# Performance work log

Hardware: AMD Instinct MI355X
Metric: run time of the kernel (lower is better)

## Reference

```python
import jax, jax.numpy as jnp
import numpy as np

B, T, OMNI_D, STATIC_D = 128, 1024, 32, 16
H = 64            # hidden // 2 (per-direction GRU size)
HID = 128         # hidden
PHYS_LEN, N_PHYS = 432, 5


def _gelu(x):
    return jax.nn.gelu(x, approximate=False)  # torch GELU default = exact erf


def _ln(x, g, b, eps=1e-5):
    m = jnp.mean(x, -1, keepdims=True)
    v = jnp.var(x, -1, keepdims=True)
    return (x - m) / jnp.sqrt(v + eps) * g + b


def _gru_layer(x, Wih, Whh, bih, bhh, reverse):
    # PyTorch GRU cell math; x: [B,T,D] -> (outputs [B,T,H], h_final [B,H])
    Hh = Whh.shape[1]
    gi = jnp.einsum('btd,gd->btg', x, Wih) + bih  # precompute input projections
    if reverse:
        gi = gi[:, ::-1]
    gi = jnp.swapaxes(gi, 0, 1)  # [T,B,3H]
    h0 = jnp.zeros((x.shape[0], Hh), x.dtype)

    def step(h, g):
        gh = h @ Whh.T + bhh
        r = jax.nn.sigmoid(g[:, :Hh] + gh[:, :Hh])
        z = jax.nn.sigmoid(g[:, Hh:2 * Hh] + gh[:, Hh:2 * Hh])
        n = jnp.tanh(g[:, 2 * Hh:] + r * gh[:, 2 * Hh:])
        hn = (1 - z) * n + z * h
        return hn, hn

    hT, ys = jax.lax.scan(step, h0, gi)
    ys = jnp.swapaxes(ys, 0, 1)
    if reverse:
        ys = ys[:, ::-1]
    return ys, hT


def _conv1d(x, W, b, pad, dil):
    y = jax.lax.conv_general_dilated(x, W, (1,), [(pad, pad)], rhs_dilation=(dil,),
                                     dimension_numbers=('NCH', 'OIH', 'NCH'))
    return y + b[None, :, None]


def setup_inputs():
    key = jax.random.key(0)
    ks = iter(jax.random.split(key, 64))

    def rn(shape, s=0.05):
        return jax.random.normal(next(ks), shape, jnp.float32) * s

    inp = {
        'omni_seq': rn((B, T, OMNI_D), 1.0),
        'static_x': rn((B, STATIC_D), 1.0),
        'phys': rn((B, N_PHYS, PHYS_LEN), 1.0),
    }
    for l, d_in in (('l0', OMNI_D), ('l1', 2 * H)):
        for dr in ('f', 'b'):
            inp[f'gru_Wih_{l}{dr}'] = rn((3 * H, d_in))
            inp[f'gru_Whh_{l}{dr}'] = rn((3 * H, H))
            inp[f'gru_bih_{l}{dr}'] = rn((3 * H,))
            inp[f'gru_bhh_{l}{dr}'] = rn((3 * H,))
    inp['sm_W'] = rn((H, STATIC_D)); inp['sm_b'] = rn((H,))
    inp['sm_ln_g'] = jnp.ones((H,), jnp.float32); inp['sm_ln_b'] = jnp.zeros((H,), jnp.float32)
    inp['gate_W'] = rn((N_PHYS, H)); inp['gate_b'] = rn((N_PHYS,))
    inp['attn_in_W'] = rn((3 * N_PHYS, N_PHYS)); inp['attn_in_b'] = rn((3 * N_PHYS,))
    inp['attn_out_W'] = rn((N_PHYS, N_PHYS)); inp['attn_out_b'] = rn((N_PHYS,))
    for i, ksz in ((1, 3), (2, 5), (3, 9)):
        inp[f'conv{i}_W'] = rn((HID // 4, N_PHYS, ksz)); inp[f'conv{i}_b'] = rn((HID // 4,))
    FUSED = HID + H + 3 * (HID // 4)  # 288
    inp['head_ln_g'] = jnp.ones((FUSED,), jnp.float32); inp['head_ln_b'] = jnp.zeros((FUSED,), jnp.float32)
    inp['head_W1'] = rn((HID, FUSED)); inp['head_b1'] = rn((HID,))
    inp['head_W2'] = rn((PHYS_LEN, HID)); inp['head_b2'] = rn((PHYS_LEN,))
    return inp


def reference(omni_seq, static_x, phys,
              gru_Wih_l0f, gru_Whh_l0f, gru_bih_l0f, gru_bhh_l0f,
              gru_Wih_l0b, gru_Whh_l0b, gru_bih_l0b, gru_bhh_l0b,
              gru_Wih_l1f, gru_Whh_l1f, gru_bih_l1f, gru_bhh_l1f,
              gru_Wih_l1b, gru_Whh_l1b, gru_bih_l1b, gru_bhh_l1b,
              sm_W, sm_b, sm_ln_g, sm_ln_b, gate_W, gate_b,
              attn_in_W, attn_in_b, attn_out_W, attn_out_b,
              conv1_W, conv1_b, conv2_W, conv2_b, conv3_W, conv3_b,
              head_ln_g, head_ln_b, head_W1, head_b1, head_W2, head_b2):
    # --- bidirectional 2-layer GRU (eval mode: dropout off) ---
    y0f, _ = _gru_layer(omni_seq, gru_Wih_l0f, gru_Whh_l0f, gru_bih_l0f, gru_bhh_l0f, False)
    y0b, _ = _gru_layer(omni_seq, gru_Wih_l0b, gru_Whh_l0b, gru_bih_l0b, gru_bhh_l0b, True)
    x1 = jnp.concatenate([y0f, y0b], -1)
    _, hf = _gru_layer(x1, gru_Wih_l1f, gru_Whh_l1f, gru_bih_l1f, gru_bhh_l1f, False)
    _, hb = _gru_layer(x1, gru_Wih_l1b, gru_Whh_l1b, gru_bih_l1b, gru_bhh_l1b, True)
    omni_embed = jnp.concatenate([hf, hb], -1)  # h_omni[-2] ++ h_omni[-1], [B,128]
    # --- static MLP ---
    static_embed = _ln(_gelu(static_x @ sm_W.T + sm_b), sm_ln_g, sm_ln_b)  # [B,64]
    # --- gating on phys channels ---
    gates = jax.nn.sigmoid(static_embed @ gate_W.T + gate_b)[..., None]  # [B,5,1]
    p = phys * gates  # [B,5,432]
    # --- tiny MHA: embed_dim=5, 5 heads, head_dim=1 -> scale = 1/sqrt(1) = 1 ---
    pt = jnp.swapaxes(p, 1, 2)  # [B,432,5]
    qkv = pt @ attn_in_W.T + attn_in_b
    E = N_PHYS
    q, k, v = qkv[..., :E], qkv[..., E:2 * E], qkv[..., 2 * E:]
    scores = jnp.einsum('bih,bjh->bhij', q, k)  # [B,5,432,432]
    attn = jax.nn.softmax(scores, -1)
    ao = jnp.einsum('bhij,bjh->bih', attn, v)
    ao = ao @ attn_out_W.T + attn_out_b  # out_proj
    p = jnp.swapaxes(ao, 1, 2)  # [B,5,432]
    # --- dilated conv branches + GELU + adaptive avg pool (= mean over length) ---
    c1 = _gelu(_conv1d(p, conv1_W, conv1_b, 1, 1)).mean(-1)
    c2 = _gelu(_conv1d(p, conv2_W, conv2_b, 2, 2)).mean(-1)
    c3 = _gelu(_conv1d(p, conv3_W, conv3_b, 4, 4)).mean(-1)
    fused = jnp.concatenate([omni_embed, static_embed, c1, c2, c3], 1)  # [B,288]
    h = _ln(fused, head_ln_g, head_ln_b)
    h = _gelu(h @ head_W1.T + head_b1)  # dropout off in eval
    return h @ head_W2.T + head_b2  # [B,432]
```

## Files before the change

kernel.cpp:

```cpp
#include <hip/hip_runtime.h>
#include <stdint.h>

#define B_ 128
#define T_ 1024
#define BT_ (B_*T_)
#define H_ 64
#define G_ 192
#define PL_ 432
#define NP_ 5
#define FUSED_ 288
#define N_IN 41
#define NSTATIC 128

typedef unsigned short u16;
typedef __attribute__((ext_vector_type(8))) short bf16x8;
typedef __attribute__((ext_vector_type(4))) float f32x4;
typedef _Float16 h2 __attribute__((ext_vector_type(2)));
typedef _Float16 h8 __attribute__((ext_vector_type(8)));

__device__ inline float bf2f(u16 u){ union{float f; unsigned int i;} c; c.i = ((unsigned int)u)<<16; return c.f; }
__device__ inline u16 f2bf(float f){ unsigned int u = __float_as_uint(f); unsigned int r = (u + 0x7fffu + ((u>>16)&1u))>>16; return (u16)r; }
__device__ inline _Float16 bf2h(u16 u){ return (_Float16)bf2f(u); }
__device__ inline float sigm(float x){ return 1.f/(1.f+__expf(-x)); }
__device__ inline float tanh_(float x){ float t = __expf(fminf(fmaxf(2.f*x,-30.f),30.f)); return (t-1.f)/(t+1.f); }
__device__ inline float gelu_(float x){ return 0.5f*x*(1.f + erff(x*0.70710678118654752f)); }
__device__ inline float wredsum(float v){
  #pragma unroll
  for(int o=32;o>0;o>>=1) v += __shfl_xor(v,o);
  return v;
}

#if __has_builtin(__builtin_amdgcn_fdot2)
__device__ inline float dot2(h2 a, h2 b, float c){ return __builtin_amdgcn_fdot2(a, b, c, false); }
#else
__device__ inline float dot2(h2 a, h2 b, float c){ return c + (float)a.x*(float)b.x + (float)a.y*(float)b.y; }
#endif

struct CvtArgs {
  const void* src[N_IN];
  unsigned dstOff[N_IN];
  unsigned cnt[N_IN];
  unsigned blkStart[N_IN+1];
};

__global__ __launch_bounds__(256) void convert_k(CvtArgs a, u16* __restrict__ dst){
  const bool isbf = (((const u16*)a.src[21])[0] == 0x3F80u);
  int b = blockIdx.x;
  int lo = 0, hi = N_IN;
  while (hi - lo > 1){ int mid = (lo+hi)>>1; if (a.blkStart[mid] <= (unsigned)b) lo = mid; else hi = mid; }
  const int i = lo;
  const unsigned lb = (unsigned)b - a.blkStart[i];
  const unsigned n = a.cnt[i];
  u16* d = dst + a.dstOff[i];
  if (isbf){
    const u16* s = (const u16*)a.src[i];
    #pragma unroll
    for(int e=0;e<8;e++){ unsigned idx = lb*2048u + e*256u + threadIdx.x; if (idx < n) d[idx] = s[idx]; }
  } else {
    const float* s = (const float*)a.src[i];
    #pragma unroll
    for(int e=0;e<8;e++){ unsigned idx = lb*2048u + e*256u + threadIdx.x; if (idx < n) d[idx] = f2bf(s[idx]); }
  }
}

__global__ __launch_bounds__(256) void gi_gemm0(const void* __restrict__ Araw,
    const u16* __restrict__ Wf, const u16* __restrict__ Wb,
    const u16* __restrict__ biasF, const u16* __restrict__ biasB,
    u16* __restrict__ out, const u16* __restrict__ detect)
{
  const bool isbf = (detect[0] == 0x3F80u);
  const int wv = threadIdx.x >> 6, lane = threadIdx.x & 63;
  const int l15 = lane & 15, quad = lane >> 4;
  const size_t mBase = (size_t)blockIdx.x*64 + wv*16;

  bf16x8 afr;
  if (isbf){
    afr = *(const bf16x8*)((const u16*)Araw + (mBase + l15)*32 + quad*8);
  } else {
    const float* af = (const float*)Araw + (mBase + l15)*32 + quad*8;
    float4 f0 = *(const float4*)af;
    float4 f1 = *(const float4*)(af+4);
    union { bf16x8 v; u16 e[8]; } u_;
    u_.e[0]=f2bf(f0.x); u_.e[1]=f2bf(f0.y); u_.e[2]=f2bf(f0.z); u_.e[3]=f2bf(f0.w);
    u_.e[4]=f2bf(f1.x); u_.e[5]=f2bf(f1.y); u_.e[6]=f2bf(f1.z); u_.e[7]=f2bf(f1.w);
    afr = u_.v;
  }

  #pragma unroll
  for(int half=0; half<2; ++half){
    const u16* W    = half ? Wb : Wf;
    const u16* bias = half ? biasB : biasF;
    u16* o = out + (size_t)half * BT_ * G_;
    for(int nt=0; nt<12; ++nt){
      int n = nt*16 + l15;
      f32x4 acc = {0.f,0.f,0.f,0.f};
      bf16x8 bfr = *(const bf16x8*)(W + n*32 + quad*8);
      acc = __builtin_amdgcn_mfma_f32_16x16x32_bf16(bfr, afr, acc, 0,0,0);
      ushort4 bb = *(const ushort4*)(bias + nt*16 + quad*4);
      ushort4 pk;
      pk.x = f2bf(acc[0] + bf2f(bb.x));
      pk.y = f2bf(acc[1] + bf2f(bb.y));
      pk.z = f2bf(acc[2] + bf2f(bb.z));
      pk.w = f2bf(acc[3] + bf2f(bb.w));
      *(ushort4*)(o + (mBase + l15)*G_ + nt*16 + quad*4) = pk;
    }
  }
}

__global__ __launch_bounds__(64)
__attribute__((amdgpu_waves_per_eu(1,1)))
void recur(const u16* __restrict__ gi,
    const u16* __restrict__ WhF, const u16* __restrict__ WhB,
    const u16* __restrict__ bhF, const u16* __restrict__ bhB,
    u16* __restrict__ y_x1, float* __restrict__ hfin, int layer)
{
  const int chain = blockIdx.x;
  const int dir = chain >> 7;
  const int b = chain & 127;
  const int j = threadIdx.x;
  const u16* Wh = dir ? WhB : WhF;
  const u16* bh = dir ? bhB : bhF;

  h2 wr[32], wz[32], wn[32];
  #pragma unroll
  for(int k8=0;k8<8;k8++){
    uint4 q;
    q = *(const uint4*)(Wh + (size_t)j*64 + k8*8);
    wr[4*k8+0] = (h2){bf2h((u16)(q.x&0xffffu)), bf2h((u16)(q.x>>16))};
    wr[4*k8+1] = (h2){bf2h((u16)(q.y&0xffffu)), bf2h((u16)(q.y>>16))};
    wr[4*k8+2] = (h2){bf2h((u16)(q.z&0xffffu)), bf2h((u16)(q.z>>16))};
    wr[4*k8+3] = (h2){bf2h((u16)(q.w&0xffffu)), bf2h((u16)(q.w>>16))};
    q = *(const uint4*)(Wh + (size_t)(64+j)*64 + k8*8);
    wz[4*k8+0] = (h2){bf2h((u16)(q.x&0xffffu)), bf2h((u16)(q.x>>16))};
    wz[4*k8+1] = (h2){bf2h((u16)(q.y&0xffffu)), bf2h((u16)(q.y>>16))};
    wz[4*k8+2] = (h2){bf2h((u16)(q.z&0xffffu)), bf2h((u16)(q.z>>16))};
    wz[4*k8+3] = (h2){bf2h((u16)(q.w&0xffffu)), bf2h((u16)(q.w>>16))};
    q = *(const uint4*)(Wh + (size_t)(128+j)*64 + k8*8);
    wn[4*k8+0] = (h2){bf2h((u16)(q.x&0xffffu)), bf2h((u16)(q.x>>16))};
    wn[4*k8+1] = (h2){bf2h((u16)(q.y&0xffffu)), bf2h((u16)(q.y>>16))};
    wn[4*k8+2] = (h2){bf2h((u16)(q.z&0xffffu)), bf2h((u16)(q.z>>16))};
    wn[4*k8+3] = (h2){bf2h((u16)(q.w&0xffffu)), bf2h((u16)(q.w>>16))};
  }
  const float bhr = bf2f(bh[j]), bhz = bf2f(bh[64+j]), bhn = bf2f(bh[128+j]);

  __shared__ __align__(16) u16 giLds[2][3072];
  __shared__ _Float16 hSf[64];
  h8* hS8 = (h8*)hSf;
  hSf[j] = (_Float16)0.f;

  const u16* giC = gi + (size_t)chain * T_ * G_;

  auto issue_chunk = [&](int c, int buf){
    int tbase = dir ? (1008 - c*16) : (c*16);
    const u16* src = giC + (size_t)tbase*G_ + j*8;
    u16* dst = &giLds[buf][0];
    #pragma unroll
    for(int i=0;i<6;i++){
      __builtin_amdgcn_global_load_lds(
        (const __attribute__((address_space(1))) void*)(src + i*512),
        (__attribute__((address_space(3))) void*)(dst + i*512), 16, 0, 0);
    }
  };

  issue_chunk(0, 0);

  float h = 0.f;
  for(int c=0; c<64; ++c){
    asm volatile("s_waitcnt vmcnt(0)" ::: "memory");
    if (c < 63) issue_chunk(c+1, (c+1)&1);
    const u16* gbuf = &giLds[c&1][0];
    #pragma unroll 2
    for(int ls=0; ls<16; ++ls){
      int row = dir ? (15-ls) : ls;
      const u16* rowp = gbuf + row*G_;
      float r0=bhr, r1=0.f, z0=bhz, z1=0.f, n0=bhn, n1=0.f;
      #pragma unroll
      for(int k=0;k<8;k++){
        h8 hv = hS8[k];
        h2 p0 = __builtin_shufflevector(hv, hv, 0, 1);
        h2 p1 = __builtin_shufflevector(hv, hv, 2, 3);
        h2 p2 = __builtin_shufflevector(hv, hv, 4, 5);
        h2 p3 = __builtin_shufflevector(hv, hv, 6, 7);
        r0 = dot2(wr[4*k+0], p0, r0); r1 = dot2(wr[4*k+1], p1, r1);
        r0 = dot2(wr[4*k+2], p2, r0); r1 = dot2(wr[4*k+3], p3, r1);
        z0 = dot2(wz[4*k+0], p0, z0); z1 = dot2(wz[4*k+1], p1, z1);
        z0 = dot2(wz[4*k+2], p2, z0); z1 = dot2(wz[4*k+3], p3, z1);
        n0 = dot2(wn[4*k+0], p0, n0); n1 = dot2(wn[4*k+1], p1, n1);
        n0 = dot2(wn[4*k+2], p2, n0); n1 = dot2(wn[4*k+3], p3, n1);
      }
      float gr = bf2f(rowp[j]), gz = bf2f(rowp[64+j]), gn = bf2f(rowp[128+j]);

      float r  = sigm(gr + (r0+r1));
      float z  = sigm(gz + (z0+z1));
      float nn = tanh_(gn + r*(n0+n1));
      h = (1.f - z)*nn + z*h;

      hSf[j] = (_Float16)h;

      if (layer == 0){
        int s = c*16 + ls;
        int t = dir ? (T_-1-s) : s;
        y_x1[((size_t)b*T_ + t)*128 + dir*64 + j] = f2bf(h);
      }
    }
  }
  if (layer == 1) hfin[b*FUSED_ + dir*64 + j] = h;
}

template<int KS, int DIL, int PAD>
__device__ inline void do_conv(const float* pS, const u16* Wc, const u16* bc,
                               float* fused, int b, int o, int p, int cslot)
{
  const int Lout = PL_ + 2*PAD - DIL*(KS-1);
  float w[5][KS];
  #pragma unroll
  for(int i=0;i<5;i++)
    #pragma unroll
    for(int t=0;t<KS;t++) w[i][t] = bf2f(Wc[(o*5+i)*KS + t]);
  float bias = bf2f(bc[o]);
  float acc = 0.f;
  for(int l=p; l<Lout; l+=8){
    float s = bias;
    #pragma unroll
    for(int t=0;t<KS;t++){
      int idx = l - PAD + t*DIL;
      if (idx >= 0 && idx < PL_){
        #pragma unroll
        for(int i=0;i<5;i++) s += w[i][t]*pS[i*PL_ + idx];
      }
    }
    acc += gelu_(s);
  }
  #pragma unroll
  for(int off=1;off<8;off<<=1) acc += __shfl_xor(acc,off);
  if (p == 0) fused[b*FUSED_ + 192 + cslot*32 + o] = acc/(float)Lout;
}

__device__ void static_body(int b, int tid,
   const u16* sx, const u16* smW, const u16* smb,
   const u16* lng, const u16* lnb, const u16* gW, const u16* gb,
   const void* physRaw, const u16* aW, const u16* ab,
   const u16* oW, const u16* ob,
   const u16* W1c, const u16* b1c, const u16* W2c, const u16* b2c,
   const u16* W3c, const u16* b3c,
   float* fused, bool isbf)
{
  __shared__ float qS[15*PL_];
  __shared__ float aoS[PL_*5];
  __shared__ float gS[5];
  __shared__ float redS[40];
  __shared__ float kmS[5], knS[5];

  if (tid < 64){
    int j = tid;
    float acc = bf2f(smb[j]);
    #pragma unroll
    for(int k=0;k<16;k++) acc += bf2f(sx[b*16+k])*bf2f(smW[j*16+k]);
    float xg = gelu_(acc);
    float m = wredsum(xg)*(1.f/64.f);
    float d = xg - m;
    float v = wredsum(d*d)*(1.f/64.f);
    float se = d*rsqrtf(v+1e-5f)*bf2f(lng[j]) + bf2f(lnb[j]);
    fused[b*FUSED_ + 128 + j] = se;
    #pragma unroll
    for(int i=0;i<5;i++){
      float p = se*bf2f(gW[i*64+j]);
      float s = wredsum(p);
      if (j == 0) gS[i] = sigm(s + bf2f(gb[i]));
    }
  }
  __syncthreads();

  for(int l=tid; l<PL_; l+=256){
    float pv[5];
    #pragma unroll
    for(int i=0;i<5;i++){
      size_t idx = ((size_t)b*5+i)*PL_ + l;
      float pr = isbf ? bf2f(((const u16*)physRaw)[idx]) : ((const float*)physRaw)[idx];
      pv[i] = pr * gS[i];
    }
    #pragma unroll
    for(int c=0;c<15;c++){
      float a = bf2f(ab[c]);
      #pragma unroll
      for(int i=0;i<5;i++) a += pv[i]*bf2f(aW[c*5+i]);
      qS[c*PL_ + l] = a;
    }
  }
  __syncthreads();

  float mx[5], mn[5];
  #pragma unroll
  for(int h=0;h<5;h++){ mx[h]=-1e30f; mn[h]=1e30f; }
  for(int jj=tid; jj<PL_; jj+=256){
    #pragma unroll
    for(int h=0;h<5;h++){ float kv=qS[(5+h)*PL_+jj]; mx[h]=fmaxf(mx[h],kv); mn[h]=fminf(mn[h],kv); }
  }
  #pragma unroll
  for(int o=32;o>0;o>>=1){
    #pragma unroll
    for(int h=0;h<5;h++){ mx[h]=fmaxf(mx[h],__shfl_xor(mx[h],o)); mn[h]=fminf(mn[h],__shfl_xor(mn[h],o)); }
  }
  int wv = tid>>6;
  if ((tid&63)==0){
    #pragma unroll
    for(int h=0;h<5;h++){ redS[wv*10+h]=mx[h]; redS[wv*10+5+h]=mn[h]; }
  }
  __syncthreads();
  if (tid < 5){
    float a=redS[tid], c=redS[5+tid];
    for(int w2=1;w2<4;w2++){ a=fmaxf(a,redS[w2*10+tid]); c=fminf(c,redS[w2*10+5+tid]); }
    kmS[tid]=a; knS[tid]=c;
  }
  __syncthreads();

  for(int i=tid; i<PL_; i+=256){
    #pragma unroll
    for(int h=0;h<5;h++){
      float s = qS[h*PL_+i];
      float m = fmaxf(s*kmS[h], s*knS[h]);
      const float* kR = &qS[(5+h)*PL_];
      const float* vR = &qS[(10+h)*PL_];
      float den=0.f, num=0.f;
      #pragma unroll 4
      for(int j2=0;j2<PL_;j2++){
        float e = __expf(s*kR[j2]-m);
        den += e; num += e*vR[j2];
      }
      aoS[i*5+h] = num/den;
    }
  }
  __syncthreads();

  float* pS = qS;
  for(int l=tid; l<PL_; l+=256){
    float a[5];
    #pragma unroll
    for(int hh=0;hh<5;hh++) a[hh] = aoS[l*5+hh];
    #pragma unroll
    for(int c=0;c<5;c++){
      float s = bf2f(ob[c]);
      #pragma unroll
      for(int hh=0;hh<5;hh++) s += a[hh]*bf2f(oW[c*5+hh]);
      pS[c*PL_ + l] = s;
    }
  }
  __syncthreads();

  int o = tid >> 3, p = tid & 7;
  do_conv<3,1,1>(pS, W1c, b1c, fused, b, o, p, 0);
  do_conv<5,2,2>(pS, W2c, b2c, fused, b, o, p, 1);
  do_conv<9,4,4>(pS, W3c, b3c, fused, b, o, p, 2);
}

__global__ __launch_bounds__(256) void gemm128_static_k(const u16* __restrict__ A,
    const u16* __restrict__ Wf, const u16* __restrict__ Wb,
    const u16* __restrict__ biasF, const u16* __restrict__ biasB,
    u16* __restrict__ out,
    const u16* __restrict__ sx, const u16* __restrict__ smW, const u16* __restrict__ smb,
    const u16* __restrict__ lng, const u16* __restrict__ lnb,
    const u16* __restrict__ gW, const u16* __restrict__ gb,
    const void* __restrict__ physRaw, const u16* __restrict__ aW, const u16* __restrict__ ab,
    const u16* __restrict__ oW, const u16* __restrict__ ob,
    const u16* __restrict__ W1c, const u16* __restrict__ b1c,
    const u16* __restrict__ W2c, const u16* __restrict__ b2c,
    const u16* __restrict__ W3c, const u16* __restrict__ b3c,
    float* __restrict__ fused, const u16* __restrict__ detect)
{
  const bool isbf = (detect[0] == 0x3F80u);
  if (blockIdx.x < NSTATIC){
    static_body(blockIdx.x, threadIdx.x, sx, smW, smb, lng, lnb, gW, gb,
                physRaw, aW, ab, oW, ob, W1c, b1c, W2c, b2c, W3c, b3c,
                fused, isbf);
    return;
  }
  const int bid = blockIdx.x - NSTATIC;
  const int wv = threadIdx.x >> 6, lane = threadIdx.x & 63;
  const int l15 = lane & 15, quad = lane >> 4;
  const size_t mBase = (size_t)bid*64 + wv*16;

  bf16x8 afr[4];
  #pragma unroll
  for(int kc=0;kc<4;kc++)
    afr[kc] = *(const bf16x8*)(A + (mBase + l15)*128 + kc*32 + quad*8);

  #pragma unroll
  for(int half=0; half<2; ++half){
    const u16* W    = half ? Wb : Wf;
    const u16* bias = half ? biasB : biasF;
    u16* o = out + (size_t)half * BT_ * G_;
    for(int nt=0; nt<12; ++nt){
      int n = nt*16 + l15;
      f32x4 acc = {0.f,0.f,0.f,0.f};
      #pragma unroll
      for(int kc=0;kc<4;kc++){
        bf16x8 bfr = *(const bf16x8*)(W + n*128 + kc*32 + quad*8);
        acc = __builtin_amdgcn_mfma_f32_16x16x32_bf16(bfr, afr[kc], acc, 0,0,0);
      }
      ushort4 bb = *(const ushort4*)(bias + nt*16 + quad*4);
      ushort4 pk;
      pk.x = f2bf(acc[0] + bf2f(bb.x));
      pk.y = f2bf(acc[1] + bf2f(bb.y));
      pk.z = f2bf(acc[2] + bf2f(bb.z));
      pk.w = f2bf(acc[3] + bf2f(bb.w));
      *(ushort4*)(o + (mBase + l15)*G_ + nt*16 + quad*4) = pk;
    }
  }
}

__global__ __launch_bounds__(448) void head_k(const float* __restrict__ fused,
   const u16* __restrict__ lng, const u16* __restrict__ lnb,
   const u16* __restrict__ W1, const u16* __restrict__ b1,
   const u16* __restrict__ W2, const u16* __restrict__ b2,
   void* __restrict__ out, const u16* __restrict__ detect)
{
  const bool isbf = (detect[0] == 0x3F80u);
  int b = blockIdx.x, tid = threadIdx.x;
  __shared__ float fS[FUSED_];
  __shared__ float hS[128];
  __shared__ float red[32];
  float v = (tid < FUSED_) ? fused[b*FUSED_ + tid] : 0.f;
  float s1 = wredsum(v);
  float s2 = wredsum(v*v);
  int wv = tid>>6;
  if ((tid&63)==0){ red[wv]=s1; red[8+wv]=s2; }
  __syncthreads();
  if (tid==0){
    float S=0.f, SS=0.f;
    for(int i=0;i<7;i++){ S+=red[i]; SS+=red[8+i]; }
    float m = S/288.f;
    red[16]=m; red[17]=SS/288.f - m*m;
  }
  __syncthreads();
  float m = red[16], var = red[17];
  if (tid < FUSED_) fS[tid] = (v-m)*rsqrtf(var+1e-5f)*bf2f(lng[tid]) + bf2f(lnb[tid]);
  __syncthreads();
  if (tid < 128){
    float a = bf2f(b1[tid]);
    const u16* wr = W1 + (size_t)tid*FUSED_;
    #pragma unroll
    for(int k8=0;k8<36;k8++){
      uint4 q = *(const uint4*)(wr + k8*8);
      a += fS[8*k8+0]*bf2f((u16)(q.x&0xffffu)) + fS[8*k8+1]*bf2f((u16)(q.x>>16))
         + fS[8*k8+2]*bf2f((u16)(q.y&0xffffu)) + fS[8*k8+3]*bf2f((u16)(q.y>>16))
         + fS[8*k8+4]*bf2f((u16)(q.z&0xffffu)) + fS[8*k8+5]*bf2f((u16)(q.z>>16))
         + fS[8*k8+6]*bf2f((u16)(q.w&0xffffu)) + fS[8*k8+7]*bf2f((u16)(q.w>>16));
    }
    hS[tid] = gelu_(a);
  }
  __syncthreads();
  if (tid < PL_){
    float a = bf2f(b2[tid]);
    const u16* wr = W2 + (size_t)tid*128;
    #pragma unroll
    for(int k8=0;k8<16;k8++){
      uint4 q = *(const uint4*)(wr + k8*8);
      a += hS[8*k8+0]*bf2f((u16)(q.x&0xffffu)) + hS[8*k8+1]*bf2f((u16)(q.x>>16))
         + hS[8*k8+2]*bf2f((u16)(q.y&0xffffu)) + hS[8*k8+3]*bf2f((u16)(q.y>>16))
         + hS[8*k8+4]*bf2f((u16)(q.z&0xffffu)) + hS[8*k8+5]*bf2f((u16)(q.z>>16))
         + hS[8*k8+6]*bf2f((u16)(q.w&0xffffu)) + hS[8*k8+7]*bf2f((u16)(q.w>>16));
    }
    size_t oi = (size_t)b*PL_ + tid;
    if (isbf) ((u16*)out)[oi] = f2bf(a);
    else      ((float*)out)[oi] = a;
  }
}

extern "C" void kernel_launch(void* const* d_in, const int* in_sizes, int n_in,
                              void* d_out, int out_size, void* d_ws, size_t ws_size,
                              hipStream_t stream)
{
  static const unsigned cnts[N_IN] = {
    4194304, 2048, 276480,
    6144, 12288, 192, 192,
    6144, 12288, 192, 192,
    24576, 12288, 192, 192,
    24576, 12288, 192, 192,
    1024, 64, 64, 64,
    320, 5,
    75, 15,
    25, 5,
    480, 32, 800, 32, 1440, 32,
    288, 288,
    36864, 128, 55296, 432
  };

  char* ws = (char*)d_ws;
  size_t off = 0;
  auto alloc = [&](size_t bytes){ size_t o = off; off = (off + bytes + 255) & ~(size_t)255; return o; };

  CvtArgs ca;
  const u16* cin[N_IN];
  unsigned totalBlocks = 0;
  for (int i=0;i<N_IN;i++){
    ca.src[i] = d_in[i];
    ca.cnt[i] = cnts[i];
    size_t o = alloc((size_t)cnts[i]*2);
    ca.dstOff[i] = (unsigned)(o/2);
    cin[i] = (const u16*)(ws + o);
    ca.blkStart[i] = totalBlocks;
    if (i != 0 && i != 2) totalBlocks += (cnts[i] + 2047u)/2048u;
  }
  ca.blkStart[N_IN] = totalBlocks;
  u16* canon = (u16*)ws;

  u16*   gi    = (u16*)  (ws + alloc((size_t)2*BT_*G_*2));
  u16*   x1    = (u16*)  (ws + alloc((size_t)BT_*128*2));
  float* fused = (float*)(ws + alloc((size_t)B_*FUSED_*4));
  (void)ws_size; (void)in_sizes; (void)n_in; (void)out_size;

  convert_k<<<totalBlocks, 256, 0, stream>>>(ca, canon);

  gi_gemm0<<<BT_/64, 256, 0, stream>>>(d_in[0], cin[3], cin[7], cin[5], cin[9], gi,
                                       (const u16*)d_in[21]);
  recur<<<256, 64, 0, stream>>>(gi, cin[4], cin[8], cin[6], cin[10], x1, nullptr, 0);
  gemm128_static_k<<<BT_/64 + NSTATIC, 256, 0, stream>>>(x1,
      cin[11], cin[15], cin[13], cin[17], gi,
      cin[1], cin[19], cin[20], cin[21], cin[22], cin[23], cin[24],
      d_in[2], cin[25], cin[26],
      cin[27], cin[28], cin[29], cin[30], cin[31], cin[32], cin[33], cin[34],
      fused, (const u16*)d_in[21]);
  recur<<<256, 64, 0, stream>>>(gi, cin[12], cin[16], cin[14], cin[18], nullptr, fused, 1);
  head_k<<<128, 448, 0, stream>>>(fused, cin[35], cin[36], cin[37], cin[38], cin[39], cin[40],
                                  d_out, (const u16*)d_in[21]);
}
```

Before: 1.233 ms.

## Fuse GI GEMMs with GRU recurrence kernels using per-tile ready flags

Merges each layer's input-projection GEMM and its recurrence into one launch. Recurrence blocks spin on per-(batch, 64-step tile) flags that the GEMM blocks publish with release stores, so the sequential scan can start before the whole GEMM finishes. GEMM tiles are issued alternately from both ends of the sequence so forward and backward chains get their first tiles early. The static/phys branch is folded into the layer-1 launch, and the flags are cleared in the convert kernel. This relies on co-residency of spinning recurrence blocks with producer blocks, and 256-thread blocks now run the 64-thread recurrence with three idle waves.

```diff
diff --git a/kernel.cpp b/kernel.cpp
--- a/kernel.cpp
+++ b/kernel.cpp
@@ -11,6 +11,8 @@
 #define FUSED_ 288
 #define N_IN 41
 #define NSTATIC 128
+#define NRECUR 256
+#define NGEMM 2048
 
 typedef unsigned short u16;
 typedef __attribute__((ext_vector_type(8))) short bf16x8;
@@ -43,9 +45,16 @@
   unsigned blkStart[N_IN+1];
 };
 
-__global__ __launch_bounds__(256) void convert_k(CvtArgs a, u16* __restrict__ dst){
+__global__ __launch_bounds__(256) void convert_k(CvtArgs a, u16* __restrict__ dst,
+                                                 unsigned* __restrict__ flags){
+  int b = blockIdx.x;
+  if ((unsigned)b >= a.blkStart[N_IN]){
+    unsigned base = ((unsigned)b - a.blkStart[N_IN])*2048u;
+    #pragma unroll
+    for(int e=0;e<8;e++){ unsigned idx = base + e*256u + threadIdx.x; if (idx < 4096u) flags[idx] = 0u; }
+    return;
+  }
   const bool isbf = (((const u16*)a.src[21])[0] == 0x3F80u);
-  int b = blockIdx.x;
   int lo = 0, hi = N_IN;
   while (hi - lo > 1){ int mid = (lo+hi)>>1; if (a.blkStart[mid] <= (unsigned)b) lo = mid; else hi = mid; }
   const int i = lo;
@@ -63,58 +72,13 @@
   }
 }
 
-__global__ __launch_bounds__(256) void gi_gemm0(const void* __restrict__ Araw,
-    const u16* __restrict__ Wf, const u16* __restrict__ Wb,
-    const u16* __restrict__ biasF, const u16* __restrict__ biasB,
-    u16* __restrict__ out, const u16* __restrict__ detect)
-{
-  const bool isbf = (detect[0] == 0x3F80u);
-  const int wv = threadIdx.x >> 6, lane = threadIdx.x & 63;
-  const int l15 = lane & 15, quad = lane >> 4;
-  const size_t mBase = (size_t)blockIdx.x*64 + wv*16;
-
-  bf16x8 afr;
-  if (isbf){
-    afr = *(const bf16x8*)((const u16*)Araw + (mBase + l15)*32 + quad*8);
-  } else {
-    const float* af = (const float*)Araw + (mBase + l15)*32 + quad*8;
-    float4 f0 = *(const float4*)af;
-    float4 f1 = *(const float4*)(af+4);
-    union { bf16x8 v; u16 e[8]; } u_;
-    u_.e[0]=f2bf(f0.x); u_.e[1]=f2bf(f0.y); u_.e[2]=f2bf(f0.z); u_.e[3]=f2bf(f0.w);
-    u_.e[4]=f2bf(f1.x); u_.e[5]=f2bf(f1.y); u_.e[6]=f2bf(f1.z); u_.e[7]=f2bf(f1.w);
-    afr = u_.v;
-  }
-
-  #pragma unroll
-  for(int half=0; half<2; ++half){
-    const u16* W    = half ? Wb : Wf;
-    const u16* bias = half ? biasB : biasF;
-    u16* o = out + (size_t)half * BT_ * G_;
-    for(int nt=0; nt<12; ++nt){
-      int n = nt*16 + l15;
-      f32x4 acc = {0.f,0.f,0.f,0.f};
-      bf16x8 bfr = *(const bf16x8*)(W + n*32 + quad*8);
-      acc = __builtin_amdgcn_mfma_f32_16x16x32_bf16(bfr, afr, acc, 0,0,0);
-      ushort4 bb = *(const ushort4*)(bias + nt*16 + quad*4);
-      ushort4 pk;
-      pk.x = f2bf(acc[0] + bf2f(bb.x));
-      pk.y = f2bf(acc[1] + bf2f(bb.y));
-      pk.z = f2bf(acc[2] + bf2f(bb.z));
-      pk.w = f2bf(acc[3] + bf2f(bb.w));
-      *(ushort4*)(o + (mBase + l15)*G_ + nt*16 + quad*4) = pk;
-    }
-  }
-}
-
-__global__ __launch_bounds__(64)
-__attribute__((amdgpu_waves_per_eu(1,1)))
-void recur(const u16* __restrict__ gi,
+template<int LAYER>
+__device__ void recur_body(int chain, const u16* gi,
     const u16* __restrict__ WhF, const u16* __restrict__ WhB,
     const u16* __restrict__ bhF, const u16* __restrict__ bhB,
-    u16* __restrict__ y_x1, float* __restrict__ hfin, int layer)
-{
-  const int chain = blockIdx.x;
+    u16* __restrict__ y_x1, float* __restrict__ hfin,
+    const unsigned* flags)
+{
   const int dir = chain >> 7;
   const int b = chain & 127;
   const int j = threadIdx.x;
@@ -162,10 +126,23 @@
     }
   };
 
+  int readyTile = -1;
+  auto wait_tile = [&](int c){
+    int tbase = dir ? (1008 - c*16) : (c*16);
+    int tile = tbase >> 6;
+    if (tile == readyTile) return;
+    const unsigned* f = &flags[b*16 + tile];
+    while (__hip_atomic_load(f, __ATOMIC_ACQUIRE, __HIP_MEMORY_SCOPE_AGENT) == 0u)
+      __builtin_amdgcn_s_sleep(2);
+    readyTile = tile;
+  };
+
+  wait_tile(0);
   issue_chunk(0, 0);
 
   float h = 0.f;
   for(int c=0; c<64; ++c){
+    if (c < 63) wait_tile(c+1);
     asm volatile("s_waitcnt vmcnt(0)" ::: "memory");
     if (c < 63) issue_chunk(c+1, (c+1)&1);
     const u16* gbuf = &giLds[c&1][0];
@@ -197,14 +174,81 @@
 
       hSf[j] = (_Float16)h;
 
-      if (layer == 0){
+      if (LAYER == 0){
         int s = c*16 + ls;
         int t = dir ? (T_-1-s) : s;
         y_x1[((size_t)b*T_ + t)*128 + dir*64 + j] = f2bf(h);
       }
     }
   }
-  if (layer == 1) hfin[b*FUSED_ + dir*64 + j] = h;
+  if (LAYER == 1) hfin[b*FUSED_ + dir*64 + j] = h;
+}
+
+__device__ inline int tile_order(int tslot){ return (tslot & 1) ? (15 - (tslot >> 1)) : (tslot >> 1); }
+
+__device__ inline void publish_flag(unsigned* flags, int idx){
+  __syncthreads();
+  if (threadIdx.x == 0){
+    __threadfence();
+    __hip_atomic_store(&flags[idx], 1u, __ATOMIC_RELEASE, __HIP_MEMORY_SCOPE_AGENT);
+  }
+}
+
+__global__ __launch_bounds__(256,1) void fused0_k(
+    const void* __restrict__ Araw,
+    const u16* __restrict__ Wf, const u16* __restrict__ Wb,
+    const u16* __restrict__ biasF, const u16* __restrict__ biasB,
+    u16* gi,
+    const u16* __restrict__ WhF, const u16* __restrict__ WhB,
+    const u16* __restrict__ bhF, const u16* __restrict__ bhB,
+    u16* __restrict__ y_x1, unsigned* flags, const u16* __restrict__ detect)
+{
+  if (blockIdx.x < NRECUR){
+    if (threadIdx.x < 64)
+      recur_body<0>(blockIdx.x, gi, WhF, WhB, bhF, bhB, y_x1, nullptr, flags);
+    return;
+  }
+  const bool isbf = (detect[0] == 0x3F80u);
+  const int g = blockIdx.x - NRECUR;
+  const int bb = g & 127;
+  const int ttile = tile_order(g >> 7);
+  const int wv = threadIdx.x >> 6, lane = threadIdx.x & 63;
+  const int l15 = lane & 15, quad = lane >> 4;
+  const size_t mBase = ((size_t)bb*16 + ttile)*64 + wv*16;
+
+  bf16x8 afr;
+  if (isbf){
+    afr = *(const bf16x8*)((const u16*)Araw + (mBase + l15)*32 + quad*8);
+  } else {
+    const float* af = (const float*)Araw + (mBase + l15)*32 + quad*8;
+    float4 f0 = *(const float4*)af;
+    float4 f1 = *(const float4*)(af+4);
+    union { bf16x8 v; u16 e[8]; } u_;
+    u_.e[0]=f2bf(f0.x); u_.e[1]=f2bf(f0.y); u_.e[2]=f2bf(f0.z); u_.e[3]=f2bf(f0.w);
+    u_.e[4]=f2bf(f1.x); u_.e[5]=f2bf(f1.y); u_.e[6]=f2bf(f1.z); u_.e[7]=f2bf(f1.w);
+    afr = u_.v;
+  }
+
+  #pragma unroll
+  for(int half=0; half<2; ++half){
+    const u16* W    = half ? Wb : Wf;
+    const u16* bias = half ? biasB : biasF;
+    u16* o = gi + (size_t)half * BT_ * G_;
+    for(int nt=0; nt<12; ++nt){
+      int n = nt*16 + l15;
+      f32x4 acc = {0.f,0.f,0.f,0.f};
+      bf16x8 bfr = *(const bf16x8*)(W + n*32 + quad*8);
+      acc = __builtin_amdgcn_mfma_f32_16x16x32_bf16(bfr, afr, acc, 0,0,0);
+      ushort4 bb4 = *(const ushort4*)(bias + nt*16 + quad*4);
+      ushort4 pk;
+      pk.x = f2bf(acc[0] + bf2f(bb4.x));
+      pk.y = f2bf(acc[1] + bf2f(bb4.y));
+      pk.z = f2bf(acc[2] + bf2f(bb4.z));
+      pk.w = f2bf(acc[3] + bf2f(bb4.w));
+      *(ushort4*)(o + (mBase + l15)*G_ + nt*16 + quad*4) = pk;
+    }
+  }
+  publish_flag(flags, bb*16 + ttile);
 }
 
 template<int KS, int DIL, int PAD>
@@ -353,10 +397,14 @@
   do_conv<9,4,4>(pS, W3c, b3c, fused, b, o, p, 2);
 }
 
-__global__ __launch_bounds__(256) void gemm128_static_k(const u16* __restrict__ A,
+__global__ __launch_bounds__(256,1) void fused1_k(
+    const u16* __restrict__ A,
     const u16* __restrict__ Wf, const u16* __restrict__ Wb,
     const u16* __restrict__ biasF, const u16* __restrict__ biasB,
-    u16* __restrict__ out,
+    u16* gi,
+    const u16* __restrict__ WhF, const u16* __restrict__ WhB,
+    const u16* __restrict__ bhF, const u16* __restrict__ bhB,
+    float* __restrict__ fusedOut, unsigned* flags,
     const u16* __restrict__ sx, const u16* __restrict__ smW, const u16* __restrict__ smb,
     const u16* __restrict__ lng, const u16* __restrict__ lnb,
     const u16* __restrict__ gW, const u16* __restrict__ gb,
@@ -365,19 +413,26 @@
     const u16* __restrict__ W1c, const u16* __restrict__ b1c,
     const u16* __restrict__ W2c, const u16* __restrict__ b2c,
     const u16* __restrict__ W3c, const u16* __restrict__ b3c,
-    float* __restrict__ fused, const u16* __restrict__ detect)
+    const u16* __restrict__ detect)
 {
   const bool isbf = (detect[0] == 0x3F80u);
-  if (blockIdx.x < NSTATIC){
-    static_body(blockIdx.x, threadIdx.x, sx, smW, smb, lng, lnb, gW, gb,
-                physRaw, aW, ab, oW, ob, W1c, b1c, W2c, b2c, W3c, b3c,
-                fused, isbf);
+  if (blockIdx.x < NRECUR){
+    if (threadIdx.x < 64)
+      recur_body<1>(blockIdx.x, gi, WhF, WhB, bhF, bhB, nullptr, fusedOut, flags);
     return;
   }
-  const int bid = blockIdx.x - NSTATIC;
+  if (blockIdx.x >= NRECUR + NGEMM){
+    static_body(blockIdx.x - (NRECUR + NGEMM), threadIdx.x,
+                sx, smW, smb, lng, lnb, gW, gb, physRaw, aW, ab,
+                oW, ob, W1c, b1c, W2c, b2c, W3c, b3c, fusedOut, isbf);
+    return;
+  }
+  const int g = blockIdx.x - NRECUR;
+  const int bb = g & 127;
+  const int ttile = tile_order(g >> 7);
   const int wv = threadIdx.x >> 6, lane = threadIdx.x & 63;
   const int l15 = lane & 15, quad = lane >> 4;
-  const size_t mBase = (size_t)bid*64 + wv*16;
+  const size_t mBase = ((size_t)bb*16 + ttile)*64 + wv*16;
 
   bf16x8 afr[4];
   #pragma unroll
@@ -388,7 +443,7 @@
   for(int half=0; half<2; ++half){
     const u16* W    = half ? Wb : Wf;
     const u16* bias = half ? biasB : biasF;
-    u16* o = out + (size_t)half * BT_ * G_;
+    u16* o = gi + (size_t)half * BT_ * G_;
     for(int nt=0; nt<12; ++nt){
       int n = nt*16 + l15;
       f32x4 acc = {0.f,0.f,0.f,0.f};
@@ -397,15 +452,16 @@
         bf16x8 bfr = *(const bf16x8*)(W + n*128 + kc*32 + quad*8);
         acc = __builtin_amdgcn_mfma_f32_16x16x32_bf16(bfr, afr[kc], acc, 0,0,0);
       }
-      ushort4 bb = *(const ushort4*)(bias + nt*16 + quad*4);
+      ushort4 bb4 = *(const ushort4*)(bias + nt*16 + quad*4);
       ushort4 pk;
-      pk.x = f2bf(acc[0] + bf2f(bb.x));
-      pk.y = f2bf(acc[1] + bf2f(bb.y));
-      pk.z = f2bf(acc[2] + bf2f(bb.z));
-      pk.w = f2bf(acc[3] + bf2f(bb.w));
+      pk.x = f2bf(acc[0] + bf2f(bb4.x));
+      pk.y = f2bf(acc[1] + bf2f(bb4.y));
+      pk.z = f2bf(acc[2] + bf2f(bb4.z));
+      pk.w = f2bf(acc[3] + bf2f(bb4.w));
       *(ushort4*)(o + (mBase + l15)*G_ + nt*16 + quad*4) = pk;
     }
   }
+  publish_flag(flags, bb*16 + ttile);
 }
 
 __global__ __launch_bounds__(448) void head_k(const float* __restrict__ fused,
@@ -507,20 +563,23 @@
   u16*   gi    = (u16*)  (ws + alloc((size_t)2*BT_*G_*2));
   u16*   x1    = (u16*)  (ws + alloc((size_t)BT_*128*2));
   float* fused = (float*)(ws + alloc((size_t)B_*FUSED_*4));
+  unsigned* flags = (unsigned*)(ws + alloc((size_t)4096*4));
   (void)ws_size; (void)in_sizes; (void)n_in; (void)out_size;
 
-  convert_k<<<totalBlocks, 256, 0, stream>>>(ca, canon);
-
-  gi_gemm0<<<BT_/64, 256, 0, stream>>>(d_in[0], cin[3], cin[7], cin[5], cin[9], gi,
-                                       (const u16*)d_in[21]);
-  recur<<<256, 64, 0, stream>>>(gi, cin[4], cin[8], cin[6], cin[10], x1, nullptr, 0);
-  gemm128_static_k<<<BT_/64 + NSTATIC, 256, 0, stream>>>(x1,
+  convert_k<<<totalBlocks + 2, 256, 0, stream>>>(ca, canon, flags);
+
+  fused0_k<<<NRECUR + NGEMM, 256, 0, stream>>>(d_in[0],
+      cin[3], cin[7], cin[5], cin[9], gi,
+      cin[4], cin[8], cin[6], cin[10], x1, flags, (const u16*)d_in[21]);
+
+  fused1_k<<<NRECUR + NGEMM + NSTATIC, 256, 0, stream>>>(x1,
       cin[11], cin[15], cin[13], cin[17], gi,
+      cin[12], cin[16], cin[14], cin[18], fused, flags + 2048,
       cin[1], cin[19], cin[20], cin[21], cin[22], cin[23], cin[24],
       d_in[2], cin[25], cin[26],
       cin[27], cin[28], cin[29], cin[30], cin[31], cin[32], cin[33], cin[34],
-      fused, (const u16*)d_in[21]);
-  recur<<<256, 64, 0, stream>>>(gi, cin[12], cin[16], cin[14], cin[18], nullptr, fused, 1);
+      (const u16*)d_in[21]);
+
   head_k<<<128, 448, 0, stream>>>(fused, cin[35], cin[36], cin[37], cin[38], cin[39], cin[40],
                                   d_out, (const u16*)d_in[21]);
 }
```

New measurement: 1.414 ms. 14.7% more time.

## Fuse layer-0 GRU input projection into the recurrent kernel

Applied to the files above, without the earlier changes.

Drops the separate layer-0 input-projection GEMM. The layer-0 recurrence kernel now holds the input weights in registers and computes the input gates per timestep with fp16 dot2, streaming the raw 32-wide input (converted to fp16 in the convert kernel) instead of a precomputed 192-wide gate tensor. This removes the large intermediate gate write and read for layer 0 and one kernel launch. In exchange it adds 48 more dot2 operations per step and 48 more weight registers to the serial critical path.

```diff
diff --git a/kernel.cpp b/kernel.cpp
--- a/kernel.cpp
+++ b/kernel.cpp
@@ -21,6 +21,7 @@
 __device__ inline float bf2f(u16 u){ union{float f; unsigned int i;} c; c.i = ((unsigned int)u)<<16; return c.f; }
 __device__ inline u16 f2bf(float f){ unsigned int u = __float_as_uint(f); unsigned int r = (u + 0x7fffu + ((u>>16)&1u))>>16; return (u16)r; }
 __device__ inline _Float16 bf2h(u16 u){ return (_Float16)bf2f(u); }
+__device__ inline u16 f2h_bits(float f){ union{_Float16 h; u16 u;} c; c.h = (_Float16)f; return c.u; }
 __device__ inline float sigm(float x){ return 1.f/(1.f+__expf(-x)); }
 __device__ inline float tanh_(float x){ float t = __expf(fminf(fmaxf(2.f*x,-30.f),30.f)); return (t-1.f)/(t+1.f); }
 __device__ inline float gelu_(float x){ return 0.5f*x*(1.f + erff(x*0.70710678118654752f)); }
@@ -52,6 +53,18 @@
   const unsigned lb = (unsigned)b - a.blkStart[i];
   const unsigned n = a.cnt[i];
   u16* d = dst + a.dstOff[i];
+  if (i == 0){
+    if (isbf){
+      const u16* s = (const u16*)a.src[i];
+      #pragma unroll
+      for(int e=0;e<8;e++){ unsigned idx = lb*2048u + e*256u + threadIdx.x; if (idx < n) d[idx] = f2h_bits(bf2f(s[idx])); }
+    } else {
+      const float* s = (const float*)a.src[i];
+      #pragma unroll
+      for(int e=0;e<8;e++){ unsigned idx = lb*2048u + e*256u + threadIdx.x; if (idx < n) d[idx] = f2h_bits(s[idx]); }
+    }
+    return;
+  }
   if (isbf){
     const u16* s = (const u16*)a.src[i];
     #pragma unroll
@@ -63,63 +76,23 @@
   }
 }
 
-__global__ __launch_bounds__(256) void gi_gemm0(const void* __restrict__ Araw,
-    const u16* __restrict__ Wf, const u16* __restrict__ Wb,
-    const u16* __restrict__ biasF, const u16* __restrict__ biasB,
-    u16* __restrict__ out, const u16* __restrict__ detect)
-{
-  const bool isbf = (detect[0] == 0x3F80u);
-  const int wv = threadIdx.x >> 6, lane = threadIdx.x & 63;
-  const int l15 = lane & 15, quad = lane >> 4;
-  const size_t mBase = (size_t)blockIdx.x*64 + wv*16;
-
-  bf16x8 afr;
-  if (isbf){
-    afr = *(const bf16x8*)((const u16*)Araw + (mBase + l15)*32 + quad*8);
-  } else {
-    const float* af = (const float*)Araw + (mBase + l15)*32 + quad*8;
-    float4 f0 = *(const float4*)af;
-    float4 f1 = *(const float4*)(af+4);
-    union { bf16x8 v; u16 e[8]; } u_;
-    u_.e[0]=f2bf(f0.x); u_.e[1]=f2bf(f0.y); u_.e[2]=f2bf(f0.z); u_.e[3]=f2bf(f0.w);
-    u_.e[4]=f2bf(f1.x); u_.e[5]=f2bf(f1.y); u_.e[6]=f2bf(f1.z); u_.e[7]=f2bf(f1.w);
-    afr = u_.v;
-  }
-
-  #pragma unroll
-  for(int half=0; half<2; ++half){
-    const u16* W    = half ? Wb : Wf;
-    const u16* bias = half ? biasB : biasF;
-    u16* o = out + (size_t)half * BT_ * G_;
-    for(int nt=0; nt<12; ++nt){
-      int n = nt*16 + l15;
-      f32x4 acc = {0.f,0.f,0.f,0.f};
-      bf16x8 bfr = *(const bf16x8*)(W + n*32 + quad*8);
-      acc = __builtin_amdgcn_mfma_f32_16x16x32_bf16(bfr, afr, acc, 0,0,0);
-      ushort4 bb = *(const ushort4*)(bias + nt*16 + quad*4);
-      ushort4 pk;
-      pk.x = f2bf(acc[0] + bf2f(bb.x));
-      pk.y = f2bf(acc[1] + bf2f(bb.y));
-      pk.z = f2bf(acc[2] + bf2f(bb.z));
-      pk.w = f2bf(acc[3] + bf2f(bb.w));
-      *(ushort4*)(o + (mBase + l15)*G_ + nt*16 + quad*4) = pk;
-    }
-  }
-}
-
 __global__ __launch_bounds__(64)
 __attribute__((amdgpu_waves_per_eu(1,1)))
-void recur(const u16* __restrict__ gi,
+void recur0_k(const u16* __restrict__ x16,
+    const u16* __restrict__ WiF, const u16* __restrict__ WiB,
+    const u16* __restrict__ biF, const u16* __restrict__ biB,
     const u16* __restrict__ WhF, const u16* __restrict__ WhB,
     const u16* __restrict__ bhF, const u16* __restrict__ bhB,
-    u16* __restrict__ y_x1, float* __restrict__ hfin, int layer)
+    u16* __restrict__ y_x1)
 {
   const int chain = blockIdx.x;
   const int dir = chain >> 7;
   const int b = chain & 127;
   const int j = threadIdx.x;
   const u16* Wh = dir ? WhB : WhF;
+  const u16* Wi = dir ? WiB : WiF;
   const u16* bh = dir ? bhB : bhF;
+  const u16* bi = dir ? biB : biF;
 
   h2 wr[32], wz[32], wn[32];
   #pragma unroll
@@ -141,6 +114,136 @@
     wn[4*k8+2] = (h2){bf2h((u16)(q.z&0xffffu)), bf2h((u16)(q.z>>16))};
     wn[4*k8+3] = (h2){bf2h((u16)(q.w&0xffffu)), bf2h((u16)(q.w>>16))};
   }
+  h2 ur[16], uz[16], un[16];
+  #pragma unroll
+  for(int k4=0;k4<4;k4++){
+    uint4 q;
+    q = *(const uint4*)(Wi + (size_t)j*32 + k4*8);
+    ur[4*k4+0] = (h2){bf2h((u16)(q.x&0xffffu)), bf2h((u16)(q.x>>16))};
+    ur[4*k4+1] = (h2){bf2h((u16)(q.y&0xffffu)), bf2h((u16)(q.y>>16))};
+    ur[4*k4+2] = (h2){bf2h((u16)(q.z&0xffffu)), bf2h((u16)(q.z>>16))};
+    ur[4*k4+3] = (h2){bf2h((u16)(q.w&0xffffu)), bf2h((u16)(q.w>>16))};
+    q = *(const uint4*)(Wi + (size_t)(64+j)*32 + k4*8);
+    uz[4*k4+0] = (h2){bf2h((u16)(q.x&0xffffu)), bf2h((u16)(q.x>>16))};
+    uz[4*k4+1] = (h2){bf2h((u16)(q.y&0xffffu)), bf2h((u16)(q.y>>16))};
+    uz[4*k4+2] = (h2){bf2h((u16)(q.z&0xffffu)), bf2h((u16)(q.z>>16))};
+    uz[4*k4+3] = (h2){bf2h((u16)(q.w&0xffffu)), bf2h((u16)(q.w>>16))};
+    q = *(const uint4*)(Wi + (size_t)(128+j)*32 + k4*8);
+    un[4*k4+0] = (h2){bf2h((u16)(q.x&0xffffu)), bf2h((u16)(q.x>>16))};
+    un[4*k4+1] = (h2){bf2h((u16)(q.y&0xffffu)), bf2h((u16)(q.y>>16))};
+    un[4*k4+2] = (h2){bf2h((u16)(q.z&0xffffu)), bf2h((u16)(q.z>>16))};
+    un[4*k4+3] = (h2){bf2h((u16)(q.w&0xffffu)), bf2h((u16)(q.w>>16))};
+  }
+  const float bR  = bf2f(bh[j])     + bf2f(bi[j]);
+  const float bZ  = bf2f(bh[64+j])  + bf2f(bi[64+j]);
+  const float bhn = bf2f(bh[128+j]);
+  const float bin = bf2f(bi[128+j]);
+
+  __shared__ __align__(16) u16 xLds[2][512];
+  __shared__ _Float16 hSf[64];
+  h8* hS8 = (h8*)hSf;
+  hSf[j] = (_Float16)0.f;
+
+  const u16* xC = x16 + (size_t)b * T_ * 32;
+
+  auto issue_chunk = [&](int c, int buf){
+    int tbase = dir ? (1008 - c*16) : (c*16);
+    const u16* src = xC + (size_t)tbase*32 + j*8;
+    u16* dst = &xLds[buf][0];
+    __builtin_amdgcn_global_load_lds(
+      (const __attribute__((address_space(1))) void*)src,
+      (__attribute__((address_space(3))) void*)dst, 16, 0, 0);
+  };
+
+  issue_chunk(0, 0);
+
+  float h = 0.f;
+  for(int c=0; c<64; ++c){
+    asm volatile("s_waitcnt vmcnt(0)" ::: "memory");
+    if (c < 63) issue_chunk(c+1, (c+1)&1);
+    const u16* xbuf = &xLds[c&1][0];
+    #pragma unroll 2
+    for(int ls=0; ls<16; ++ls){
+      int row = dir ? (15-ls) : ls;
+      const h8* x8 = (const h8*)(xbuf + row*32);
+      float r0=bR, r1=0.f, z0=bZ, z1=0.f;
+      float nh0=bhn, nh1=0.f, nx0=bin, nx1=0.f;
+      #pragma unroll
+      for(int k=0;k<4;k++){
+        h8 xv = x8[k];
+        h2 q0 = __builtin_shufflevector(xv, xv, 0, 1);
+        h2 q1 = __builtin_shufflevector(xv, xv, 2, 3);
+        h2 q2 = __builtin_shufflevector(xv, xv, 4, 5);
+        h2 q3 = __builtin_shufflevector(xv, xv, 6, 7);
+        r0 = dot2(ur[4*k+0], q0, r0); r1 = dot2(ur[4*k+1], q1, r1);
+        r0 = dot2(ur[4*k+2], q2, r0); r1 = dot2(ur[4*k+3], q3, r1);
+        z0 = dot2(uz[4*k+0], q0, z0); z1 = dot2(uz[4*k+1], q1, z1);
+        z0 = dot2(uz[4*k+2], q2, z0); z1 = dot2(uz[4*k+3], q3, z1);
+        nx0 = dot2(un[4*k+0], q0, nx0); nx1 = dot2(un[4*k+1], q1, nx1);
+        nx0 = dot2(un[4*k+2], q2, nx0); nx1 = dot2(un[4*k+3], q3, nx1);
+      }
+      #pragma unroll
+      for(int k=0;k<8;k++){
+        h8 hv = hS8[k];
+        h2 p0 = __builtin_shufflevector(hv, hv, 0, 1);
+        h2 p1 = __builtin_shufflevector(hv, hv, 2, 3);
+        h2 p2 = __builtin_shufflevector(hv, hv, 4, 5);
+        h2 p3 = __builtin_shufflevector(hv, hv, 6, 7);
+        r0 = dot2(wr[4*k+0], p0, r0); r1 = dot2(wr[4*k+1], p1, r1);
+        r0 = dot2(wr[4*k+2], p2, r0); r1 = dot2(wr[4*k+3], p3, r1);
+        z0 = dot2(wz[4*k+0], p0, z0); z1 = dot2(wz[4*k+1], p1, z1);
+        z0 = dot2(wz[4*k+2], p2, z0); z1 = dot2(wz[4*k+3], p3, z1);
+        nh0 = dot2(wn[4*k+0], p0, nh0); nh1 = dot2(wn[4*k+1], p1, nh1);
+        nh0 = dot2(wn[4*k+2], p2, nh0); nh1 = dot2(wn[4*k+3], p3, nh1);
+      }
+      float r  = sigm(r0+r1);
+      float z  = sigm(z0+z1);
+      float nn = tanh_((nx0+nx1) + r*(nh0+nh1));
+      h = (1.f - z)*nn + z*h;
+
+      hSf[j] = (_Float16)h;
+
+      int s = c*16 + ls;
+      int t = dir ? (T_-1-s) : s;
+      y_x1[((size_t)b*T_ + t)*128 + dir*64 + j] = f2bf(h);
+    }
+  }
+}
+
+__global__ __launch_bounds__(64)
+__attribute__((amdgpu_waves_per_eu(1,1)))
+void recur(const u16* __restrict__ gi,
+    const u16* __restrict__ WhF, const u16* __restrict__ WhB,
+    const u16* __restrict__ bhF, const u16* __restrict__ bhB,
+    float* __restrict__ hfin)
+{
+  const int chain = blockIdx.x;
+  const int dir = chain >> 7;
+  const int b = chain & 127;
+  const int j = threadIdx.x;
+  const u16* Wh = dir ? WhB : WhF;
+  const u16* bh = dir ? bhB : bhF;
+
+  h2 wr[32], wz[32], wn[32];
+  #pragma unroll
+  for(int k8=0;k8<8;k8++){
+    uint4 q;
+    q = *(const uint4*)(Wh + (size_t)j*64 + k8*8);
+    wr[4*k8+0] = (h2){bf2h((u16)(q.x&0xffffu)), bf2h((u16)(q.x>>16))};
+    wr[4*k8+1] = (h2){bf2h((u16)(q.y&0xffffu)), bf2h((u16)(q.y>>16))};
+    wr[4*k8+2] = (h2){bf2h((u16)(q.z&0xffffu)), bf2h((u16)(q.z>>16))};
+    wr[4*k8+3] = (h2){bf2h((u16)(q.w&0xffffu)), bf2h((u16)(q.w>>16))};
+    q = *(const uint4*)(Wh + (size_t)(64+j)*64 + k8*8);
+    wz[4*k8+0] = (h2){bf2h((u16)(q.x&0xffffu)), bf2h((u16)(q.x>>16))};
+    wz[4*k8+1] = (h2){bf2h((u16)(q.y&0xffffu)), bf2h((u16)(q.y>>16))};
+    wz[4*k8+2] = (h2){bf2h((u16)(q.z&0xffffu)), bf2h((u16)(q.z>>16))};
+    wz[4*k8+3] = (h2){bf2h((u16)(q.w&0xffffu)), bf2h((u16)(q.w>>16))};
+    q = *(const uint4*)(Wh + (size_t)(128+j)*64 + k8*8);
+    wn[4*k8+0] = (h2){bf2h((u16)(q.x&0xffffu)), bf2h((u16)(q.x>>16))};
+    wn[4*k8+1] = (h2){bf2h((u16)(q.y&0xffffu)), bf2h((u16)(q.y>>16))};
+    wn[4*k8+2] = (h2){bf2h((u16)(q.z&0xffffu)), bf2h((u16)(q.z>>16))};
+    wn[4*k8+3] = (h2){bf2h((u16)(q.w&0xffffu)), bf2h((u16)(q.w>>16))};
+  }
   const float bhr = bf2f(bh[j]), bhz = bf2f(bh[64+j]), bhn = bf2f(bh[128+j]);
 
   __shared__ __align__(16) u16 giLds[2][3072];
@@ -196,15 +299,9 @@
       h = (1.f - z)*nn + z*h;
 
       hSf[j] = (_Float16)h;
-
-      if (layer == 0){
-        int s = c*16 + ls;
-        int t = dir ? (T_-1-s) : s;
-        y_x1[((size_t)b*T_ + t)*128 + dir*64 + j] = f2bf(h);
-      }
-    }
-  }
-  if (layer == 1) hfin[b*FUSED_ + dir*64 + j] = h;
+    }
+  }
+  hfin[b*FUSED_ + dir*64 + j] = h;
 }
 
 template<int KS, int DIL, int PAD>
@@ -499,7 +596,7 @@
     ca.dstOff[i] = (unsigned)(o/2);
     cin[i] = (const u16*)(ws + o);
     ca.blkStart[i] = totalBlocks;
-    if (i != 0 && i != 2) totalBlocks += (cnts[i] + 2047u)/2048u;
+    if (i != 2) totalBlocks += (cnts[i] + 2047u)/2048u;
   }
   ca.blkStart[N_IN] = totalBlocks;
   u16* canon = (u16*)ws;
@@ -511,16 +608,18 @@
 
   convert_k<<<totalBlocks, 256, 0, stream>>>(ca, canon);
 
-  gi_gemm0<<<BT_/64, 256, 0, stream>>>(d_in[0], cin[3], cin[7], cin[5], cin[9], gi,
-                                       (const u16*)d_in[21]);
-  recur<<<256, 64, 0, stream>>>(gi, cin[4], cin[8], cin[6], cin[10], x1, nullptr, 0);
+  recur0_k<<<256, 64, 0, stream>>>(cin[0], cin[3], cin[7], cin[5], cin[9],
+                                   cin[4], cin[8], cin[6], cin[10], x1);
+
   gemm128_static_k<<<BT_/64 + NSTATIC, 256, 0, stream>>>(x1,
       cin[11], cin[15], cin[13], cin[17], gi,
       cin[1], cin[19], cin[20], cin[21], cin[22], cin[23], cin[24],
       d_in[2], cin[25], cin[26],
       cin[27], cin[28], cin[29], cin[30], cin[31], cin[32], cin[33], cin[34],
       fused, (const u16*)d_in[21]);
-  recur<<<256, 64, 0, stream>>>(gi, cin[12], cin[16], cin[14], cin[18], nullptr, fused, 1);
+
+  recur<<<256, 64, 0, stream>>>(gi, cin[12], cin[16], cin[14], cin[18], fused);
+
   head_k<<<128, 448, 0, stream>>>(fused, cin[35], cin[36], cin[37], cin[38], cin[39], cin[40],
                                   d_out, (const u16*)d_in[21]);
 }
```

After: 1.219 ms, median of 2. No clear change (-1.1%).
